# Kernel optimization log

Hardware: AMD Instinct MI355X
Metric: run time of the kernel (lower is better)

Reference implementation:

```python
import jax, jax.numpy as jnp
import numpy as np

N_NODES = 100000
N_EDGES = 1600000
D = 64
L = 3


def setup_inputs() -> dict:
    key = jax.random.key(0)
    ks = jax.random.split(key, 6)
    x = jax.random.normal(ks[0], (N_NODES, D), dtype=jnp.float32)
    edge_index = jax.random.randint(ks[1], (2, N_EDGES), 0, N_NODES, dtype=jnp.int64)
    # Stacked SAGEConv params: lin_l (neighbor branch, with bias), lin_r (root branch, no bias)
    scale = 1.0 / np.sqrt(D)
    Wl = jax.random.normal(ks[2], (L, D, D), dtype=jnp.float32) * scale
    bl = jnp.zeros((L, D), dtype=jnp.float32)
    Wr = jax.random.normal(ks[3], (L, D, D), dtype=jnp.float32) * scale
    return {
        "x": x,
        "Wl": Wl,
        "bl": bl,
        "Wr": Wr,
        "edge_index": edge_index,
        "batch_size": N_NODES,
        "framework": 1,
    }


def reference(x, Wl, bl, Wr, edge_index, batch_size, framework):
    src, dst = edge_index[0], edge_index[1]
    n = x.shape[0]
    # in-degree for mean aggregation; isolated nodes -> divide by 1 (result stays 0)
    deg = jax.ops.segment_sum(jnp.ones((src.shape[0],), dtype=x.dtype), dst, num_segments=n)
    inv_deg = (1.0 / jnp.maximum(deg, 1.0))[:, None]  # [N,1]
    for i in range(Wl.shape[0]):
        msg = x[src]                                              # [E, D] gather
        agg = jax.ops.segment_sum(msg, dst, num_segments=n) * inv_deg  # [N, D] mean
        x = jax.nn.relu(agg @ Wl[i].T + bl[i] + x @ Wr[i].T)
    if framework:
        return x
    return x[:batch_size]
```

## Files before the change

kernel.cpp:

```cpp
#include <hip/hip_runtime.h>
#include <hip/hip_bf16.h>


#define D 64
#define KDIM 128
#define TS 64
#define ASTH 136
#define BSH 9
#define BNODES 512
#define ECHUNK 8192
#define BCAP 12288

typedef unsigned long long u64;
typedef unsigned short u16;
typedef __attribute__((ext_vector_type(8))) short bf16x8;
typedef __attribute__((ext_vector_type(4))) float f32x4;

__device__ inline u16 f2bf(float f) {
    unsigned u = __float_as_uint(f);
    return (u16)((u + 0x7fffu + ((u >> 16) & 1u)) >> 16);
}
__device__ inline void bfx8_to_f(uint4 u, float* f) {
    f[0] = __uint_as_float(u.x << 16); f[1] = __uint_as_float(u.x & 0xffff0000u);
    f[2] = __uint_as_float(u.y << 16); f[3] = __uint_as_float(u.y & 0xffff0000u);
    f[4] = __uint_as_float(u.z << 16); f[5] = __uint_as_float(u.z & 0xffff0000u);
    f[6] = __uint_as_float(u.w << 16); f[7] = __uint_as_float(u.w & 0xffff0000u);
}


__global__ __launch_bounds__(256) void convert_x_kernel(
    const float* __restrict__ x, u16* __restrict__ xb, int total8)
{
    int i = blockIdx.x * 256 + threadIdx.x;
    if (i >= total8) return;
    float4 a = *(const float4*)(x + (size_t)i * 8);
    float4 b = *(const float4*)(x + (size_t)i * 8 + 4);
    uint4 o;
    o.x = (unsigned)f2bf(a.x) | ((unsigned)f2bf(a.y) << 16);
    o.y = (unsigned)f2bf(a.z) | ((unsigned)f2bf(a.w) << 16);
    o.z = (unsigned)f2bf(b.x) | ((unsigned)f2bf(b.y) << 16);
    o.w = (unsigned)f2bf(b.z) | ((unsigned)f2bf(b.w) << 16);
    *(uint4*)(xb + (size_t)i * 8) = o;
}


__global__ __launch_bounds__(256) void bin_kernel(
    const int* __restrict__ srcp, const int* __restrict__ dstp,
    int* __restrict__ bcnt, u64* __restrict__ staging,
    int nE, int nb)
{
    __shared__ int hist[1024];
    __shared__ int bbase[1024];
    int t = threadIdx.x;
    int e0 = blockIdx.x * ECHUNK;
    for (int i = t; i < nb; i += 256) hist[i] = 0;
    __syncthreads();
    int dcache[32];
#pragma unroll
    for (int j = 0; j < 32; ++j) {
        int e = e0 + j * 256 + t;
        int d = (e < nE) ? dstp[e] : -1;
        dcache[j] = d;
        if (d >= 0) atomicAdd(&hist[d >> BSH], 1);
    }
    __syncthreads();
    for (int i = t; i < nb; i += 256) {
        int c = hist[i];
        bbase[i] = (c > 0) ? atomicAdd(&bcnt[i], c) : 0;
        hist[i] = 0;
    }
    __syncthreads();
#pragma unroll
    for (int j = 0; j < 32; ++j) {
        int e = e0 + j * 256 + t;
        int d = dcache[j];
        if (d >= 0) {
            int b = d >> BSH;
            int pos = bbase[b] + atomicAdd(&hist[b], 1);
            u64 rec = ((u64)(unsigned)(d & (BNODES - 1)) << 32) | (unsigned)srcp[e];
            staging[(size_t)b * BCAP + pos] = rec;
        }
    }
}

__global__ __launch_bounds__(256) void bucket_build_kernel(
    const u64* __restrict__ staging, const int* __restrict__ bcnt,
    int* __restrict__ offs, float* __restrict__ inv,
    int* __restrict__ csr, int n, int nb, int E)
{
    __shared__ int hist[BNODES];
    __shared__ int loffs[BNODES + 1];
    __shared__ int cur[BNODES];
    __shared__ int sbase;
    int b = blockIdx.x, t = threadIdx.x;
    int n0 = b << BSH;
    int nodes = min(BNODES, n - n0);
    int cnt = bcnt[b];
    const u64* seg = staging + (size_t)b * BCAP;
    if (t < 64) {
        int partial = 0;
        for (int i = t; i < b; i += 64) partial += bcnt[i];
#pragma unroll
        for (int off = 32; off > 0; off >>= 1) partial += __shfl_xor(partial, off);
        if (t == 0) sbase = partial;
    }
    for (int i = t; i < nodes; i += 256) { hist[i] = 0; cur[i] = 0; }
    __syncthreads();
    int gbase = sbase;
    for (int e = t; e < cnt; e += 256) atomicAdd(&hist[(int)(seg[e] >> 32)], 1);
    __syncthreads();
    if (t < 64) {
        int carry = 0;
        for (int base0 = 0; base0 < nodes; base0 += 64) {
            int i = base0 + t;
            int v = (i < nodes) ? hist[i] : 0;
            int inc = v;
#pragma unroll
            for (int off = 1; off < 64; off <<= 1) {
                int v2 = __shfl_up(inc, off);
                if (t >= off) inc += v2;
            }
            if (i < nodes) loffs[i] = carry + (inc - v);
            carry += __shfl(inc, 63);
        }
        if (t == 0) loffs[nodes] = carry;
    }
    __syncthreads();
    for (int i = t; i < nodes; i += 256) {
        offs[n0 + i] = gbase + loffs[i];
        inv[n0 + i] = 1.0f / fmaxf((float)hist[i], 1.0f);
    }
    if (b == nb - 1 && t == 0) offs[n] = E;
    for (int e = t; e < cnt; e += 256) {
        u64 rec = seg[e];
        int dl = (int)(rec >> 32);
        int sv = (int)(rec & 0xffffffffu);
        int pos = loffs[dl] + atomicAdd(&cur[dl], 1);
        csr[gbase + pos] = sv;
    }
}

__global__ void pack_w_kernel(const float* __restrict__ Wl,
                              const float* __restrict__ Wr,
                              u16* __restrict__ wpk, int total)
{
    int idx = blockIdx.x * 256 + threadIdx.x;
    if (idx >= total) return;
    int j    = idx & 7;
    int lane = (idx >> 3) & 63;
    int nt   = (idx >> 9) & 3;
    int kt   = (idx >> 11) & 3;
    int l    = idx >> 13;
    int k = kt * 32 + (lane >> 4) * 8 + j;
    int n = nt * 16 + (lane & 15);
    float v = (k < D) ? Wl[((l * D) + n) * D + k]
                      : Wr[((l * D) + n) * D + (k - D)];
    wpk[idx] = f2bf(v);
}


template <int WRITE_F32>
__global__ __launch_bounds__(512, 6) void layer_kernel(
    const u16* __restrict__ xin, const int* __restrict__ offs,
    const int* __restrict__ csr, const float* __restrict__ inv,
    const u16* __restrict__ wpk,
    const float* __restrict__ bl,
    void* __restrict__ outp, int n)
{
    __shared__ u16 A[TS * ASTH];
    const int t = threadIdx.x, w = t >> 6, lane = t & 63;
    const int sub = lane >> 3;
    const int fl  = lane & 7;
    const int base = lane & 56;
    const int v0 = blockIdx.x * TS;

    const int r = w * 8 + sub;
    const int v = v0 + r;
    int s = 0, e = 0;
    float scale = 0.f;
    uint4 xv = make_uint4(0, 0, 0, 0);
    if (v < n) {
        s = offs[v];
        e = offs[v + 1];
        scale = inv[v];
        xv = *(const uint4*)(xin + (size_t)v * D + fl * 8);
    }
    float acc[8] = {};
    int idx = 0;
    if (s + fl < e) idx = csr[s + fl];
    while (__any(s < e)) {
        int cnt = e - s;
        cnt = cnt < 0 ? 0 : (cnt > 8 ? 8 : cnt);
        int idxv[8];
#pragma unroll
        for (int j = 0; j < 8; ++j) idxv[j] = __shfl(idx, base + j);
        uint4 rows[8];
#pragma unroll
        for (int j = 0; j < 8; ++j)
            rows[j] = *(const uint4*)(xin + (size_t)idxv[j] * D + fl * 8);
        int s2 = s + 8;
        idx = 0;
        if (s2 + fl < e) idx = csr[s2 + fl];
#pragma unroll
        for (int j = 0; j < 8; ++j) {
            float f[8];
            bfx8_to_f(rows[j], f);
            float m = (j < cnt) ? 1.f : 0.f;
#pragma unroll
            for (int q = 0; q < 8; ++q) acc[q] = fmaf(f[q], m, acc[q]);
        }
        s = s2;
    }
    uint4 o;
    o.x = (unsigned)f2bf(acc[0] * scale) | ((unsigned)f2bf(acc[1] * scale) << 16);
    o.y = (unsigned)f2bf(acc[2] * scale) | ((unsigned)f2bf(acc[3] * scale) << 16);
    o.z = (unsigned)f2bf(acc[4] * scale) | ((unsigned)f2bf(acc[5] * scale) << 16);
    o.w = (unsigned)f2bf(acc[6] * scale) | ((unsigned)f2bf(acc[7] * scale) << 16);
    *(uint4*)(&A[r * ASTH + fl * 8]) = o;
    *(uint4*)(&A[r * ASTH + D + fl * 8]) = xv;
    __syncthreads();

    const int m = lane & 15, quad = lane >> 4;
    const int row16 = (w >> 1) * 16;
    const int ntb = (w & 1) * 2;
    f32x4 cacc[2];
    cacc[0] = (f32x4){0.f, 0.f, 0.f, 0.f};
    cacc[1] = (f32x4){0.f, 0.f, 0.f, 0.f};
#pragma unroll
    for (int kt = 0; kt < 4; ++kt) {
        bf16x8 af = *(const bf16x8*)(&A[(row16 + m) * ASTH + kt * 32 + quad * 8]);
#pragma unroll
        for (int ntl = 0; ntl < 2; ++ntl) {
            bf16x8 bf = *(const bf16x8*)(wpk + (size_t)((kt * 4 + ntb + ntl) * 64 + lane) * 8);
            cacc[ntl] = __builtin_amdgcn_mfma_f32_16x16x32_bf16(af, bf, cacc[ntl], 0, 0, 0);
        }
    }
#pragma unroll
    for (int ntl = 0; ntl < 2; ++ntl) {
        int col = (ntb + ntl) * 16 + m;
        float bias = bl[col];
#pragma unroll
        for (int reg = 0; reg < 4; ++reg) {
            int row = row16 + quad * 4 + reg;
            int vv = v0 + row;
            if (vv < n) {
                float val = fmaxf(cacc[ntl][reg] + bias, 0.f);
                if (WRITE_F32)
                    ((float*)outp)[(size_t)vv * D + col] = val;
                else
                    ((u16*)outp)[(size_t)vv * D + col] = f2bf(val);
            }
        }
    }
}


extern "C" void kernel_launch(void* const* d_in, const int* in_sizes, int n_in,
                              void* d_out, int out_size, void* d_ws, size_t ws_size,
                              hipStream_t stream)
{
    const float* x  = (const float*)d_in[0];
    const float* Wl = (const float*)d_in[1];
    const float* bl = (const float*)d_in[2];
    const float* Wr = (const float*)d_in[3];
    const int*   ei = (const int*)d_in[4];

    const int N = in_sizes[0] / D;
    const int E = in_sizes[4] / 2;
    const int L = in_sizes[1] / (D * D);

    const int* srcp = ei;
    const int* dstp = ei + E;

    const int nbuck = (N + BNODES - 1) >> BSH;

    char* w = (char*)d_ws;
    int* bcnt  = (int*)w;               w += 1024 * sizeof(int);
    int* offs  = (int*)w;               w += (size_t)(N + 1) * sizeof(int);
    w = (char*)(((uintptr_t)w + 15) & ~(uintptr_t)15);
    float* inv = (float*)w;             w += (size_t)N * sizeof(float);
    w = (char*)(((uintptr_t)w + 15) & ~(uintptr_t)15);
    int* csr   = (int*)w;               w += (size_t)E * sizeof(int);
    w = (char*)(((uintptr_t)w + 15) & ~(uintptr_t)15);
    u16* wpk   = (u16*)w;               w += (size_t)L * 8192 * sizeof(u16);
    w = (char*)(((uintptr_t)w + 15) & ~(uintptr_t)15);
    u16* xbf0  = (u16*)w;               w += (size_t)N * D * sizeof(u16);
    w = (char*)(((uintptr_t)w + 15) & ~(uintptr_t)15);
    u16* xbf1  = (u16*)w;               w += (size_t)N * D * sizeof(u16);
    w = (char*)(((uintptr_t)w + 15) & ~(uintptr_t)15);
    u16* xbf2  = (u16*)w;               w += (size_t)N * D * sizeof(u16);
    w = (char*)(((uintptr_t)w + 15) & ~(uintptr_t)15);
    u64* staging = (u64*)w;

    hipMemsetAsync(bcnt, 0, 1024 * sizeof(int), stream);

    convert_x_kernel<<<(N * D / 8 + 255) / 256, 256, 0, stream>>>(x, xbf0, N * D / 8);
    bin_kernel<<<(E + ECHUNK - 1) / ECHUNK, 256, 0, stream>>>(srcp, dstp, bcnt, staging, E, nbuck);
    bucket_build_kernel<<<nbuck, 256, 0, stream>>>(staging, bcnt, offs, inv, csr, N, nbuck, E);

    int wtotal = L * 8192;
    pack_w_kernel<<<(wtotal + 255) / 256, 256, 0, stream>>>(Wl, Wr, wpk, wtotal);

    const int nblk = (N + TS - 1) / TS;
    const u16* xcur = xbf0;
    for (int i = 0; i < L; ++i) {
        const u16* wpl = wpk + (size_t)i * 8192;
        const float* bll = bl + (size_t)i * D;
        if (i == L - 1) {
            layer_kernel<1><<<nblk, 512, 0, stream>>>(xcur, offs, csr, inv, wpl, bll, d_out, N);
        } else {
            u16* xdst = (i & 1) ? xbf2 : xbf1;
            layer_kernel<0><<<nblk, 512, 0, stream>>>(xcur, offs, csr, inv, wpl, bll, xdst, N);
            xcur = xdst;
        }
    }
}
```

Baseline: 298.1 us.

## Split layer into degree-sorted gather and separate GEMM kernel

Each layer is split into a gather kernel and a GEMM kernel. The gather kernel processes nodes in an order sorted by in-degree within each bucket, using a permutation built in bucket_build, so that the 8 nodes sharing a wave have similar edge counts and less divergence in the neighbor loop. The aggregated rows go to a bf16 buffer that reuses the staging area, and a separate MFMA GEMM kernel reads them back. The x conversion and weight packing are merged into one setup kernel, and the bucket and chunk sizes are halved. The cost is an extra N×D bf16 write and read per layer plus one more launch per layer.

```diff
diff --git a/kernel.cpp b/kernel.cpp
--- a/kernel.cpp
+++ b/kernel.cpp
@@ -6,10 +6,10 @@
 #define KDIM 128
 #define TS 64
 #define ASTH 136
-#define BSH 9
-#define BNODES 512
-#define ECHUNK 8192
-#define BCAP 12288
+#define BSH 8
+#define BNODES 256
+#define ECHUNK 4096
+#define BCAP 5120
 
 typedef unsigned long long u64;
 typedef unsigned short u16;
@@ -27,20 +27,36 @@
     f[6] = __uint_as_float(u.w << 16); f[7] = __uint_as_float(u.w & 0xffff0000u);
 }
 
-
-__global__ __launch_bounds__(256) void convert_x_kernel(
-    const float* __restrict__ x, u16* __restrict__ xb, int total8)
-{
-    int i = blockIdx.x * 256 + threadIdx.x;
-    if (i >= total8) return;
-    float4 a = *(const float4*)(x + (size_t)i * 8);
-    float4 b = *(const float4*)(x + (size_t)i * 8 + 4);
-    uint4 o;
-    o.x = (unsigned)f2bf(a.x) | ((unsigned)f2bf(a.y) << 16);
-    o.y = (unsigned)f2bf(a.z) | ((unsigned)f2bf(a.w) << 16);
-    o.z = (unsigned)f2bf(b.x) | ((unsigned)f2bf(b.y) << 16);
-    o.w = (unsigned)f2bf(b.z) | ((unsigned)f2bf(b.w) << 16);
-    *(uint4*)(xb + (size_t)i * 8) = o;
+__global__ __launch_bounds__(256) void setup_kernel(
+    const float* __restrict__ x, u16* __restrict__ xb, int total8,
+    const float* __restrict__ Wl, const float* __restrict__ Wr,
+    u16* __restrict__ wpk, int wtotal)
+{
+    int gid = blockIdx.x * 256 + threadIdx.x;
+    if (gid < total8) {
+        float4 a = *(const float4*)(x + (size_t)gid * 8);
+        float4 b = *(const float4*)(x + (size_t)gid * 8 + 4);
+        uint4 o;
+        o.x = (unsigned)f2bf(a.x) | ((unsigned)f2bf(a.y) << 16);
+        o.y = (unsigned)f2bf(a.z) | ((unsigned)f2bf(a.w) << 16);
+        o.z = (unsigned)f2bf(b.x) | ((unsigned)f2bf(b.y) << 16);
+        o.w = (unsigned)f2bf(b.z) | ((unsigned)f2bf(b.w) << 16);
+        *(uint4*)(xb + (size_t)gid * 8) = o;
+    } else {
+        int idx = gid - total8;
+        if (idx < wtotal) {
+            int j    = idx & 7;
+            int lane = (idx >> 3) & 63;
+            int nt   = (idx >> 9) & 3;
+            int kt   = (idx >> 11) & 3;
+            int l    = idx >> 13;
+            int k = kt * 32 + (lane >> 4) * 8 + j;
+            int n = nt * 16 + (lane & 15);
+            float v = (k < D) ? Wl[((l * D) + n) * D + k]
+                              : Wr[((l * D) + n) * D + (k - D)];
+            wpk[idx] = f2bf(v);
+        }
+    }
 }
 
 
@@ -55,9 +71,9 @@
     int e0 = blockIdx.x * ECHUNK;
     for (int i = t; i < nb; i += 256) hist[i] = 0;
     __syncthreads();
-    int dcache[32];
-#pragma unroll
-    for (int j = 0; j < 32; ++j) {
+    int dcache[16];
+#pragma unroll
+    for (int j = 0; j < 16; ++j) {
         int e = e0 + j * 256 + t;
         int d = (e < nE) ? dstp[e] : -1;
         dcache[j] = d;
@@ -71,7 +87,7 @@
     }
     __syncthreads();
 #pragma unroll
-    for (int j = 0; j < 32; ++j) {
+    for (int j = 0; j < 16; ++j) {
         int e = e0 + j * 256 + t;
         int d = dcache[j];
         if (d >= 0) {
@@ -85,12 +101,15 @@
 
 __global__ __launch_bounds__(256) void bucket_build_kernel(
     const u64* __restrict__ staging, const int* __restrict__ bcnt,
-    int* __restrict__ offs, float* __restrict__ inv,
+    int* __restrict__ offs, float* __restrict__ inv, int* __restrict__ perm,
     int* __restrict__ csr, int n, int nb, int E)
 {
     __shared__ int hist[BNODES];
     __shared__ int loffs[BNODES + 1];
     __shared__ int cur[BNODES];
+    __shared__ int dhist[64];
+    __shared__ int dbase[64];
+    __shared__ int dcur[64];
     __shared__ int sbase;
     int b = blockIdx.x, t = threadIdx.x;
     int n0 = b << BSH;
@@ -105,10 +124,12 @@
         if (t == 0) sbase = partial;
     }
     for (int i = t; i < nodes; i += 256) { hist[i] = 0; cur[i] = 0; }
+    if (t < 64) { dhist[t] = 0; dcur[t] = 0; }
     __syncthreads();
     int gbase = sbase;
     for (int e = t; e < cnt; e += 256) atomicAdd(&hist[(int)(seg[e] >> 32)], 1);
     __syncthreads();
+    for (int i = t; i < nodes; i += 256) atomicAdd(&dhist[min(hist[i], 63)], 1);
     if (t < 64) {
         int carry = 0;
         for (int base0 = 0; base0 < nodes; base0 += 64) {
@@ -126,11 +147,27 @@
         if (t == 0) loffs[nodes] = carry;
     }
     __syncthreads();
+    if (t < 64) {
+        int v = dhist[t];
+        int inc = v;
+#pragma unroll
+        for (int off = 1; off < 64; off <<= 1) {
+            int v2 = __shfl_up(inc, off);
+            if (t >= off) inc += v2;
+        }
+        dbase[t] = inc - v;
+    }
     for (int i = t; i < nodes; i += 256) {
         offs[n0 + i] = gbase + loffs[i];
         inv[n0 + i] = 1.0f / fmaxf((float)hist[i], 1.0f);
     }
     if (b == nb - 1 && t == 0) offs[n] = E;
+    __syncthreads();
+    for (int i = t; i < nodes; i += 256) {
+        int bin = min(hist[i], 63);
+        int pos = dbase[bin] + atomicAdd(&dcur[bin], 1);
+        perm[n0 + pos] = n0 + i;
+    }
     for (int e = t; e < cnt; e += 256) {
         u64 rec = seg[e];
         int dl = (int)(rec >> 32);
@@ -140,50 +177,25 @@
     }
 }
 
-__global__ void pack_w_kernel(const float* __restrict__ Wl,
-                              const float* __restrict__ Wr,
-                              u16* __restrict__ wpk, int total)
-{
-    int idx = blockIdx.x * 256 + threadIdx.x;
-    if (idx >= total) return;
-    int j    = idx & 7;
-    int lane = (idx >> 3) & 63;
-    int nt   = (idx >> 9) & 3;
-    int kt   = (idx >> 11) & 3;
-    int l    = idx >> 13;
-    int k = kt * 32 + (lane >> 4) * 8 + j;
-    int n = nt * 16 + (lane & 15);
-    float v = (k < D) ? Wl[((l * D) + n) * D + k]
-                      : Wr[((l * D) + n) * D + (k - D)];
-    wpk[idx] = f2bf(v);
-}
-
-
-template <int WRITE_F32>
-__global__ __launch_bounds__(512, 6) void layer_kernel(
+
+__global__ __launch_bounds__(256, 6) void gather_kernel(
     const u16* __restrict__ xin, const int* __restrict__ offs,
     const int* __restrict__ csr, const float* __restrict__ inv,
-    const u16* __restrict__ wpk,
-    const float* __restrict__ bl,
-    void* __restrict__ outp, int n)
-{
-    __shared__ u16 A[TS * ASTH];
+    const int* __restrict__ perm, u16* __restrict__ agg, int n)
+{
     const int t = threadIdx.x, w = t >> 6, lane = t & 63;
     const int sub = lane >> 3;
     const int fl  = lane & 7;
     const int base = lane & 56;
-    const int v0 = blockIdx.x * TS;
-
-    const int r = w * 8 + sub;
-    const int v = v0 + r;
-    int s = 0, e = 0;
+    const int r = (blockIdx.x * 4 + w) * 8 + sub;
+
+    int v = -1, s = 0, e = 0;
     float scale = 0.f;
-    uint4 xv = make_uint4(0, 0, 0, 0);
-    if (v < n) {
+    if (r < n) {
+        v = perm[r];
         s = offs[v];
         e = offs[v + 1];
         scale = inv[v];
-        xv = *(const uint4*)(xin + (size_t)v * D + fl * 8);
     }
     float acc[8] = {};
     int idx = 0;
@@ -211,13 +223,37 @@
         }
         s = s2;
     }
-    uint4 o;
-    o.x = (unsigned)f2bf(acc[0] * scale) | ((unsigned)f2bf(acc[1] * scale) << 16);
-    o.y = (unsigned)f2bf(acc[2] * scale) | ((unsigned)f2bf(acc[3] * scale) << 16);
-    o.z = (unsigned)f2bf(acc[4] * scale) | ((unsigned)f2bf(acc[5] * scale) << 16);
-    o.w = (unsigned)f2bf(acc[6] * scale) | ((unsigned)f2bf(acc[7] * scale) << 16);
-    *(uint4*)(&A[r * ASTH + fl * 8]) = o;
-    *(uint4*)(&A[r * ASTH + D + fl * 8]) = xv;
+    if (v >= 0) {
+        uint4 o;
+        o.x = (unsigned)f2bf(acc[0] * scale) | ((unsigned)f2bf(acc[1] * scale) << 16);
+        o.y = (unsigned)f2bf(acc[2] * scale) | ((unsigned)f2bf(acc[3] * scale) << 16);
+        o.z = (unsigned)f2bf(acc[4] * scale) | ((unsigned)f2bf(acc[5] * scale) << 16);
+        o.w = (unsigned)f2bf(acc[6] * scale) | ((unsigned)f2bf(acc[7] * scale) << 16);
+        *(uint4*)(agg + (size_t)v * D + fl * 8) = o;
+    }
+}
+
+
+template <int WRITE_F32>
+__global__ __launch_bounds__(512) void gemm_kernel(
+    const u16* __restrict__ agg, const u16* __restrict__ xin,
+    const u16* __restrict__ wpk,
+    const float* __restrict__ bl,
+    void* __restrict__ outp, int n)
+{
+    __shared__ u16 A[TS * ASTH];
+    const int t = threadIdx.x, w = t >> 6, lane = t & 63;
+    const int v0 = blockIdx.x * TS;
+
+    for (int i = t; i < TS * 16; i += 512) {
+        int row = i >> 4, c = i & 15;
+        int v = v0 + row;
+        uint4 val = make_uint4(0, 0, 0, 0);
+        if (v < n)
+            val = (c < 8) ? *(const uint4*)(agg + (size_t)v * D + c * 8)
+                          : *(const uint4*)(xin + (size_t)v * D + (c - 8) * 8);
+        *(uint4*)(&A[row * ASTH + c * 8]) = val;
+    }
     __syncthreads();
 
     const int m = lane & 15, quad = lane >> 4;
@@ -280,6 +316,8 @@
     w = (char*)(((uintptr_t)w + 15) & ~(uintptr_t)15);
     float* inv = (float*)w;             w += (size_t)N * sizeof(float);
     w = (char*)(((uintptr_t)w + 15) & ~(uintptr_t)15);
+    int* perm  = (int*)w;               w += (size_t)N * sizeof(int);
+    w = (char*)(((uintptr_t)w + 15) & ~(uintptr_t)15);
     int* csr   = (int*)w;               w += (size_t)E * sizeof(int);
     w = (char*)(((uintptr_t)w + 15) & ~(uintptr_t)15);
     u16* wpk   = (u16*)w;               w += (size_t)L * 8192 * sizeof(u16);
@@ -291,26 +329,29 @@
     u16* xbf2  = (u16*)w;               w += (size_t)N * D * sizeof(u16);
     w = (char*)(((uintptr_t)w + 15) & ~(uintptr_t)15);
     u64* staging = (u64*)w;
+    u16* aggb = (u16*)staging;
 
     hipMemsetAsync(bcnt, 0, 1024 * sizeof(int), stream);
 
-    convert_x_kernel<<<(N * D / 8 + 255) / 256, 256, 0, stream>>>(x, xbf0, N * D / 8);
+    int total8 = N * D / 8;
+    int wtotal = L * 8192;
+    setup_kernel<<<(total8 + wtotal + 255) / 256, 256, 0, stream>>>(
+        x, xbf0, total8, Wl, Wr, wpk, wtotal);
     bin_kernel<<<(E + ECHUNK - 1) / ECHUNK, 256, 0, stream>>>(srcp, dstp, bcnt, staging, E, nbuck);
-    bucket_build_kernel<<<nbuck, 256, 0, stream>>>(staging, bcnt, offs, inv, csr, N, nbuck, E);
-
-    int wtotal = L * 8192;
-    pack_w_kernel<<<(wtotal + 255) / 256, 256, 0, stream>>>(Wl, Wr, wpk, wtotal);
-
-    const int nblk = (N + TS - 1) / TS;
+    bucket_build_kernel<<<nbuck, 256, 0, stream>>>(staging, bcnt, offs, inv, perm, csr, N, nbuck, E);
+
+    const int ngblk = ((N + 7) / 8 + 3) / 4;
+    const int nmblk = (N + TS - 1) / TS;
     const u16* xcur = xbf0;
     for (int i = 0; i < L; ++i) {
         const u16* wpl = wpk + (size_t)i * 8192;
         const float* bll = bl + (size_t)i * D;
+        gather_kernel<<<ngblk, 256, 0, stream>>>(xcur, offs, csr, inv, perm, aggb, N);
         if (i == L - 1) {
-            layer_kernel<1><<<nblk, 512, 0, stream>>>(xcur, offs, csr, inv, wpl, bll, d_out, N);
+            gemm_kernel<1><<<nmblk, 512, 0, stream>>>(aggb, xcur, wpl, bll, d_out, N);
         } else {
             u16* xdst = (i & 1) ? xbf2 : xbf1;
-            layer_kernel<0><<<nblk, 512, 0, stream>>>(xcur, offs, csr, inv, wpl, bll, xdst, N);
+            gemm_kernel<0><<<nmblk, 512, 0, stream>>>(aggb, xcur, wpl, bll, xdst, N);
             xcur = xdst;
         }
     }
```

After: 351.7 us. +18.0%, slower.
